# Optimization experiments

Hardware: AMD Instinct MI355X
Metric: run time of the kernel (lower is better)

The kernel has to match this reference:

```python
import jax, jax.numpy as jnp
import numpy as np

PARALLISM = 128          # Subarray[0]
O_BITS = 8               # ADC_resolution
SCALE = float(2 ** O_BITS - 1)          # 255.0
MAXCURRENT = 0.02 * PARALLISM           # 2.56 ; a_scale/w_scale == 2**32-1 so guards skip them


def setup_inputs() -> dict:
    key = jax.random.key(0)
    k1, k2, k3 = jax.random.split(key, 3)
    B, K, N = 8192, 4096, 4096
    x = jax.random.normal(k1, (B, K), dtype=jnp.float32) * 0.1
    weight = jax.random.normal(k2, (N, K), dtype=jnp.float32)  # torch Linear layout [out, in]
    bias = jax.random.normal(k3, (N,), dtype=jnp.float32)
    return {"x": x, "weight": weight, "bias": bias, "layer": 1}


def _quantize_partial(x):
    # output_quantize.forward: clamp to +/-maxcurrent, scale to [−scale, scale], round (STE), rescale
    y = jnp.clip(x, -MAXCURRENT, MAXCURRENT)
    y = y / MAXCURRENT * SCALE
    y = y + jax.lax.stop_gradient(jnp.round(y) - y)  # Round.apply with straight-through grad
    return y / SCALE * MAXCURRENT


def reference(x, weight, bias, layer):
    # Hard_fc: chunked VMM along the input-feature (row) dim with per-subarray ADC quantization
    B, K = x.shape
    w = weight.T                      # [K, N]
    N = w.shape[1]
    num = K // PARALLISM              # K chosen divisible by PARALLISM (32 chunks)
    xc = x.reshape(B, num, PARALLISM).swapaxes(0, 1)       # [num, B, P]
    wc = w.reshape(num, PARALLISM, N)                       # [num, P, N]

    def step(acc, chunk):
        xi, wi = chunk                # [B, P], [P, N]
        return acc + _quantize_partial(xi @ wi), None

    acc0 = jnp.zeros((B, N), dtype=x.dtype)
    out, _ = jax.lax.scan(step, acc0, (xc, wc))
    out = out + bias
    return out.reshape(B, -1)
```

## Files before the change

kernel.cpp:

```cpp
#include <hip/hip_runtime.h>


typedef __attribute__((ext_vector_type(8))) short short8;
typedef __attribute__((ext_vector_type(4))) float floatx4;

#define BM 128
#define BN 128
#define BK 64

static __device__ __forceinline__ unsigned short f2bf(float f) {
    union { float f; unsigned int u; } v; v.f = f;
    unsigned int u = v.u;
    unsigned int r = (u + 0x7fffu + ((u >> 16) & 1u)) >> 16;
    return (unsigned short)r;
}

__global__ void cast_x_kernel(const float* __restrict__ in,
                              unsigned short* __restrict__ out, int n4) {
    int i = blockIdx.x * 256 + threadIdx.x;
    if (i >= n4) return;
    float4 v = ((const float4*)in)[i];
    ushort4 o;
    o.x = f2bf(v.x); o.y = f2bf(v.y); o.z = f2bf(v.z); o.w = f2bf(v.w);
    ((ushort4*)out)[i] = o;
}

__global__ void cast_w_kernel(const float* __restrict__ in,
                              unsigned short* __restrict__ out, int n4) {
    const float s = 99.609375f;
    int i = blockIdx.x * 256 + threadIdx.x;
    if (i >= n4) return;
    float4 v = ((const float4*)in)[i];
    ushort4 o;
    o.x = f2bf(v.x * s); o.y = f2bf(v.y * s); o.z = f2bf(v.z * s); o.w = f2bf(v.w * s);
    ((ushort4*)out)[i] = o;
}

__global__ __launch_bounds__(256, 2) void vmm_kernel(
    const unsigned short* __restrict__ A,
    const unsigned short* __restrict__ Bw,
    const float* __restrict__ bias,
    float* __restrict__ out,
    int N, int K)
{
    __shared__ unsigned short sA[BM * BK];
    __shared__ unsigned short sB[BN * BK];

    const int tid  = threadIdx.x;
    const int wid  = tid >> 6;
    const int lane = tid & 63;

    const int m0 = blockIdx.y * BM;
    const int n0 = blockIdx.x * BN;

    const int waveM = (wid >> 1) * 64;
    const int waveN = (wid & 1) * 64;

    floatx4 acc[4][4];
    floatx4 macc[4][4];
    #pragma unroll
    for (int i = 0; i < 4; ++i)
        #pragma unroll
        for (int j = 0; j < 4; ++j) {
            acc[i][j]  = (floatx4){0.f, 0.f, 0.f, 0.f};
            macc[i][j] = (floatx4){0.f, 0.f, 0.f, 0.f};
        }

    const int srow = lane >> 3;
    const int scol = (lane & 7) * 8;

    const unsigned short* gA = A  + (long)m0 * K;
    const unsigned short* gB = Bw + (long)n0 * K;

    for (int k0 = 0; k0 < K; k0 += BK) {
        #pragma unroll
        for (int i = 0; i < 4; ++i) {
            const int seg = i * 4 + wid;
            const long grow = (long)(seg * 8 + srow);
            __builtin_amdgcn_global_load_lds(
                (const __attribute__((address_space(1))) void*)(gA + grow * K + k0 + scol),
                (__attribute__((address_space(3))) void*)(sA + seg * 512),
                16, 0, 0);
            __builtin_amdgcn_global_load_lds(
                (const __attribute__((address_space(1))) void*)(gB + grow * K + k0 + scol),
                (__attribute__((address_space(3))) void*)(sB + seg * 512),
                16, 0, 0);
        }
        __syncthreads();

        #pragma unroll
        for (int kk = 0; kk < BK; kk += 32) {
            const int krd = kk + (lane >> 4) * 8;
            short8 af[4], bfr[4];
            #pragma unroll
            for (int tm = 0; tm < 4; ++tm)
                af[tm] = *(const short8*)(sA + (waveM + tm * 16 + (lane & 15)) * BK + krd);
            #pragma unroll
            for (int tn = 0; tn < 4; ++tn)
                bfr[tn] = *(const short8*)(sB + (waveN + tn * 16 + (lane & 15)) * BK + krd);
            #pragma unroll
            for (int tm = 0; tm < 4; ++tm)
                #pragma unroll
                for (int tn = 0; tn < 4; ++tn)
                    acc[tm][tn] = __builtin_amdgcn_mfma_f32_16x16x32_bf16(
                        af[tm], bfr[tn], acc[tm][tn], 0, 0, 0);
        }

        if (((k0 + BK) & 127) == 0) {
            #pragma unroll
            for (int tm = 0; tm < 4; ++tm)
                #pragma unroll
                for (int tn = 0; tn < 4; ++tn) {
                    #pragma unroll
                    for (int r = 0; r < 4; ++r) {
                        float v = acc[tm][tn][r];
                        v = __builtin_amdgcn_fmed3f(v, -255.0f, 255.0f);
                        v = __builtin_rintf(v);
                        macc[tm][tn][r] += v;
                    }
                    acc[tm][tn] = (floatx4){0.f, 0.f, 0.f, 0.f};
                }
        }
        __syncthreads();
    }

    const float invs = 2.56f / 255.0f;
    #pragma unroll
    for (int tn = 0; tn < 4; ++tn) {
        const int col = n0 + waveN + tn * 16 + (lane & 15);
        const float bv = bias[col];
        #pragma unroll
        for (int tm = 0; tm < 4; ++tm) {
            const int row = m0 + waveM + tm * 16 + (lane >> 4) * 4;
            #pragma unroll
            for (int r = 0; r < 4; ++r)
                out[(long)(row + r) * N + col] = macc[tm][tn][r] * invs + bv;
        }
    }
}

extern "C" void kernel_launch(void* const* d_in, const int* in_sizes, int n_in,
                              void* d_out, int out_size, void* d_ws, size_t ws_size,
                              hipStream_t stream) {
    const float* x    = (const float*)d_in[0];
    const float* w    = (const float*)d_in[1];
    const float* bias = (const float*)d_in[2];

    const int N = in_sizes[2];
    const int K = in_sizes[1] / N;
    const int B = in_sizes[0] / K;
    float* out = (float*)d_out;

    unsigned short* xb = (unsigned short*)d_ws;
    unsigned short* wb = xb + (size_t)B * K;

    {
        int n4 = (int)(((long)B * K) / 4);
        cast_x_kernel<<<(n4 + 255) / 256, 256, 0, stream>>>(x, xb, n4);
    }
    {
        int n4 = (int)(((long)N * K) / 4);
        cast_w_kernel<<<(n4 + 255) / 256, 256, 0, stream>>>(w, wb, n4);
    }
    dim3 grid(N / BN, B / BM);
    vmm_kernel<<<grid, 256, 0, stream>>>(xb, wb, bias, out, N, K);
}
```

Measured before the change: 725.3 us.

## Swizzle LDS tiles, raise occupancy hint, and grid-stride cast kernels

XOR-swizzles the 16-byte column chunks of the shared-memory A/B tiles so the MFMA fragment reads hit different LDS banks instead of conflicting. It also raises the launch-bounds occupancy hint from 2 to 4 blocks per CU. The two cast kernels become grid-stride loops with a fixed 4096-block grid, each thread handling 4 float4s. The higher occupancy hint may force register spilling given the 32 accumulator vectors per thread, and the cast loop's access pattern has each thread handle consecutive float4s, which reduces coalescing.

```diff
diff --git a/kernel.cpp b/kernel.cpp
--- a/kernel.cpp
+++ b/kernel.cpp
@@ -16,27 +16,42 @@
 }
 
 __global__ void cast_x_kernel(const float* __restrict__ in,
-                              unsigned short* __restrict__ out, int n4) {
-    int i = blockIdx.x * 256 + threadIdx.x;
-    if (i >= n4) return;
-    float4 v = ((const float4*)in)[i];
-    ushort4 o;
-    o.x = f2bf(v.x); o.y = f2bf(v.y); o.z = f2bf(v.z); o.w = f2bf(v.w);
-    ((ushort4*)out)[i] = o;
+                              unsigned short* __restrict__ out, long n4) {
+    const long stride = (long)gridDim.x * 256 * 4;
+    for (long base = ((long)blockIdx.x * 256 + threadIdx.x) * 4; base < n4; base += stride) {
+        #pragma unroll
+        for (int j = 0; j < 4; ++j) {
+            long i = base + j;
+            if (i < n4) {
+                float4 v = ((const float4*)in)[i];
+                ushort4 o;
+                o.x = f2bf(v.x); o.y = f2bf(v.y); o.z = f2bf(v.z); o.w = f2bf(v.w);
+                ((ushort4*)out)[i] = o;
+            }
+        }
+    }
 }
 
 __global__ void cast_w_kernel(const float* __restrict__ in,
-                              unsigned short* __restrict__ out, int n4) {
+                              unsigned short* __restrict__ out, long n4) {
     const float s = 99.609375f;
-    int i = blockIdx.x * 256 + threadIdx.x;
-    if (i >= n4) return;
-    float4 v = ((const float4*)in)[i];
-    ushort4 o;
-    o.x = f2bf(v.x * s); o.y = f2bf(v.y * s); o.z = f2bf(v.z * s); o.w = f2bf(v.w * s);
-    ((ushort4*)out)[i] = o;
+    const long stride = (long)gridDim.x * 256 * 4;
+    for (long base = ((long)blockIdx.x * 256 + threadIdx.x) * 4; base < n4; base += stride) {
+        #pragma unroll
+        for (int j = 0; j < 4; ++j) {
+            long i = base + j;
+            if (i < n4) {
+                float4 v = ((const float4*)in)[i];
+                ushort4 o;
+                o.x = f2bf(v.x * s); o.y = f2bf(v.y * s);
+                o.z = f2bf(v.z * s); o.w = f2bf(v.w * s);
+                ((ushort4*)out)[i] = o;
+            }
+        }
+    }
 }
 
-__global__ __launch_bounds__(256, 2) void vmm_kernel(
+__global__ __launch_bounds__(256, 4) void vmm_kernel(
     const unsigned short* __restrict__ A,
     const unsigned short* __restrict__ Bw,
     const float* __restrict__ bias,
@@ -67,7 +82,7 @@
         }
 
     const int srow = lane >> 3;
-    const int scol = (lane & 7) * 8;
+    const int scol = (((lane & 7) ^ srow) & 7) * 8;
 
     const unsigned short* gA = A  + (long)m0 * K;
     const unsigned short* gB = Bw + (long)n0 * K;
@@ -90,14 +105,15 @@
 
         #pragma unroll
         for (int kk = 0; kk < BK; kk += 32) {
-            const int krd = kk + (lane >> 4) * 8;
+            const int lc = (kk >> 3) + (lane >> 4);
+            const int pc = (lc ^ (lane & 7)) * 8;
             short8 af[4], bfr[4];
             #pragma unroll
             for (int tm = 0; tm < 4; ++tm)
-                af[tm] = *(const short8*)(sA + (waveM + tm * 16 + (lane & 15)) * BK + krd);
+                af[tm] = *(const short8*)(sA + (waveM + tm * 16 + (lane & 15)) * BK + pc);
             #pragma unroll
             for (int tn = 0; tn < 4; ++tn)
-                bfr[tn] = *(const short8*)(sB + (waveN + tn * 16 + (lane & 15)) * BK + krd);
+                bfr[tn] = *(const short8*)(sB + (waveN + tn * 16 + (lane & 15)) * BK + pc);
             #pragma unroll
             for (int tm = 0; tm < 4; ++tm)
                 #pragma unroll
@@ -155,12 +171,12 @@
     unsigned short* wb = xb + (size_t)B * K;
 
     {
-        int n4 = (int)(((long)B * K) / 4);
-        cast_x_kernel<<<(n4 + 255) / 256, 256, 0, stream>>>(x, xb, n4);
+        long n4 = ((long)B * K) / 4;
+        cast_x_kernel<<<4096, 256, 0, stream>>>(x, xb, n4);
     }
     {
-        int n4 = (int)(((long)N * K) / 4);
-        cast_w_kernel<<<(n4 + 255) / 256, 256, 0, stream>>>(w, wb, n4);
+        long n4 = ((long)N * K) / 4;
+        cast_w_kernel<<<4096, 256, 0, stream>>>(w, wb, n4);
     }
     dim3 grid(N / BN, B / BM);
     vmm_kernel<<<grid, 256, 0, stream>>>(xb, wb, bias, out, N, K);
```

New measurement: 1.516 ms. 109% more time.
